# Performance work log

Measured on AMD Instinct MI355X. Metric: run time of the kernel, lower is better.

## Reference

```python
import jax, jax.numpy as jnp
import numpy as np

S, D, H, F = 4096, 1024, 16, 4096
DH = D // H  # 64
EPS = 1e-6


def _layer_norm(x, scale, bias):
    mu = jnp.mean(x, axis=-1, keepdims=True)
    var = jnp.mean(jnp.square(x - mu), axis=-1, keepdims=True)
    return (x - mu) * jax.lax.rsqrt(var + EPS) * scale + bias


def setup_inputs() -> dict:
    key = jax.random.key(0)
    ks = jax.random.split(key, 12)
    s = 0.02
    return {
        "x": jax.random.normal(ks[0], (S, D), jnp.float32),
        "Wq": jax.random.normal(ks[1], (D, H, DH), jnp.float32) * s,
        "bq": jnp.zeros((H, DH), jnp.float32),
        "Wk": jax.random.normal(ks[2], (D, H, DH), jnp.float32) * s,
        "bk": jnp.zeros((H, DH), jnp.float32),
        "Wv": jax.random.normal(ks[3], (D, H, DH), jnp.float32) * s,
        "bv": jnp.zeros((H, DH), jnp.float32),
        "Wo": jax.random.normal(ks[4], (H, DH, D), jnp.float32) * s,
        "bo": jnp.zeros((D,), jnp.float32),
        "ln1_scale": jnp.ones((D,), jnp.float32),
        "ln1_bias": jnp.zeros((D,), jnp.float32),
        "ln2_scale": jnp.ones((D,), jnp.float32),
        "ln2_bias": jnp.zeros((D,), jnp.float32),
        "W1": jax.random.normal(ks[5], (D, F), jnp.float32) * s,
        "b1": jnp.zeros((F,), jnp.float32),
        "W2": jax.random.normal(ks[6], (F, D), jnp.float32) * s,
        "b2": jnp.zeros((D,), jnp.float32),
    }


def reference(x, Wq, bq, Wk, bk, Wv, bv, Wo, bo,
              ln1_scale, ln1_bias, ln2_scale, ln2_bias,
              W1, b1, W2, b2):
    # --- attention block (pre-LN, no mask, no dropout, no RoPE) ---
    y = _layer_norm(x, ln1_scale, ln1_bias)            # [S, D]
    q = jnp.einsum("sd,dhk->shk", y, Wq) + bq          # [S, H, DH]
    k = jnp.einsum("sd,dhk->shk", y, Wk) + bk
    v = jnp.einsum("sd,dhk->shk", y, Wv) + bv
    scale = jnp.float32(1.0 / np.sqrt(DH))
    scores = jnp.einsum("qhd,khd->hqk", q * scale, k)  # [H, S, S]
    w = jax.nn.softmax(scores, axis=-1)
    ctx = jnp.einsum("hqk,khd->qhd", w, v)             # [S, H, DH]
    attn_out = jnp.einsum("qhd,hdo->qo", ctx, Wo) + bo  # [S, D]
    x = x + attn_out
    # --- FFN block ---
    y = _layer_norm(x, ln2_scale, ln2_bias)
    y = jax.nn.gelu(y @ W1 + b1, approximate=False)
    y = y @ W2 + b2
    return x + y
```

## Files before the change

### kernel.cpp

```cpp
#include <hip/hip_runtime.h>
#include <cstdint>
#include <cstddef>


typedef __attribute__((ext_vector_type(8))) __bf16 bf16x8;
typedef __attribute__((ext_vector_type(4))) float f32x4;
typedef __attribute__((ext_vector_type(2))) float f32x2;
typedef __attribute__((ext_vector_type(16))) float f32x16;
typedef __attribute__((ext_vector_type(4))) unsigned int u32x4;

__device__ inline unsigned short f2bf(float f) {
  unsigned int u = __float_as_uint(f);
  u += 0x7fffu + ((u >> 16) & 1u);
  return (unsigned short)(u >> 16);
}

__device__ inline void gload_lds16(const unsigned short* g, unsigned short* l) {
  __builtin_amdgcn_global_load_lds(
      (const __attribute__((address_space(1))) void*)g,
      (__attribute__((address_space(3))) void*)l, 16, 0, 0);
}

__global__ __launch_bounds__(256) void prep_all(
    const float* __restrict__ Wq, const float* __restrict__ Wk,
    const float* __restrict__ Wv, const float* __restrict__ Wo,
    const float* __restrict__ W1, const float* __restrict__ W2,
    const float* __restrict__ bq, const float* __restrict__ bk,
    const float* __restrict__ bv,
    const float* __restrict__ x, const float* __restrict__ g1,
    const float* __restrict__ be1, unsigned short* __restrict__ y1,
    unsigned short* __restrict__ WqkvT, unsigned short* __restrict__ WoT,
    unsigned short* __restrict__ W1T, unsigned short* __restrict__ W2T,
    float* __restrict__ bqkv) {
  int b = blockIdx.x;
  const int tid = threadIdx.x;
  if (b < 12) {
    int i = b * 256 + tid;
    bqkv[i] = (i < 1024) ? bq[i] : (i < 2048 ? bk[i - 1024] : bv[i - 2048]);
    return;
  }
  b -= 12;
  if (b < 4096) {
    const int row = b;
    const float4 v = ((const float4*)(x + (size_t)row * 1024))[tid];
    float s = v.x + v.y + v.z + v.w;
#pragma unroll
    for (int off = 1; off < 64; off <<= 1) s += __shfl_xor(s, off);
    __shared__ float red1[4], red2[4];
    int wave = tid >> 6;
    if ((tid & 63) == 0) red1[wave] = s;
    __syncthreads();
    float mu = (red1[0] + red1[1] + red1[2] + red1[3]) * (1.0f / 1024.0f);
    float dx = v.x - mu, dy = v.y - mu, dz = v.z - mu, dw = v.w - mu;
    float s2 = dx * dx + dy * dy + dz * dz + dw * dw;
#pragma unroll
    for (int off = 1; off < 64; off <<= 1) s2 += __shfl_xor(s2, off);
    if ((tid & 63) == 0) red2[wave] = s2;
    __syncthreads();
    float var = (red2[0] + red2[1] + red2[2] + red2[3]) * (1.0f / 1024.0f);
    float inv = rsqrtf(var + 1e-6f);
    int c = tid * 4;
    ushort4 o;
    o.x = f2bf(dx * inv * g1[c + 0] + be1[c + 0]);
    o.y = f2bf(dy * inv * g1[c + 1] + be1[c + 1]);
    o.z = f2bf(dz * inv * g1[c + 2] + be1[c + 2]);
    o.w = f2bf(dw * inv * g1[c + 3] + be1[c + 3]);
    ((ushort4*)(y1 + (size_t)row * 1024))[tid] = o;
    return;
  }
  b -= 4096;
  const float* in;
  unsigned short* out;
  int K, N, nbx;
  if (b < 4096) {
    const int sel = b >> 10;
    in = (sel == 0) ? Wq : (sel == 1) ? Wk : (sel == 2) ? Wv : Wo;
    out = (sel == 3) ? WoT : WqkvT + (size_t)sel * 1024 * 1024;
    K = 1024; N = 1024; nbx = 32; b &= 1023;
  } else if (b < 8192) {
    b -= 4096; in = W1; out = W1T; K = 1024; N = 4096; nbx = 128;
  } else {
    b -= 8192; in = W2; out = W2T; K = 4096; N = 1024; nbx = 32;
  }
  const int nb = (b % nbx) * 32, kb = (b / nbx) * 32;
  __shared__ float t[32][33];
  const int tx = tid & 31, ty = tid >> 5;
#pragma unroll
  for (int i = 0; i < 32; i += 8)
    t[ty + i][tx] = in[(size_t)(kb + ty + i) * N + nb + tx];
  __syncthreads();
#pragma unroll
  for (int i = 0; i < 32; i += 8)
    out[(size_t)(nb + ty + i) * K + kb + tx] = f2bf(t[tx][ty + i]);
}

__global__ __launch_bounds__(256) void ln_kernel(const float* __restrict__ x,
                                                 const float* __restrict__ gamma,
                                                 const float* __restrict__ beta,
                                                 unsigned short* __restrict__ y) {
  int row = blockIdx.x, tid = threadIdx.x;
  const float4 v = ((const float4*)(x + (size_t)row * 1024))[tid];
  float s = v.x + v.y + v.z + v.w;
#pragma unroll
  for (int off = 1; off < 64; off <<= 1) s += __shfl_xor(s, off);
  __shared__ float red1[4], red2[4];
  int wave = tid >> 6;
  if ((tid & 63) == 0) red1[wave] = s;
  __syncthreads();
  float mu = (red1[0] + red1[1] + red1[2] + red1[3]) * (1.0f / 1024.0f);
  float dx = v.x - mu, dy = v.y - mu, dz = v.z - mu, dw = v.w - mu;
  float s2 = dx * dx + dy * dy + dz * dz + dw * dw;
#pragma unroll
  for (int off = 1; off < 64; off <<= 1) s2 += __shfl_xor(s2, off);
  if ((tid & 63) == 0) red2[wave] = s2;
  __syncthreads();
  float var = (red2[0] + red2[1] + red2[2] + red2[3]) * (1.0f / 1024.0f);
  float inv = rsqrtf(var + 1e-6f);
  int c = tid * 4;
  ushort4 o;
  o.x = f2bf(dx * inv * gamma[c + 0] + beta[c + 0]);
  o.y = f2bf(dy * inv * gamma[c + 1] + beta[c + 1]);
  o.z = f2bf(dz * inv * gamma[c + 2] + beta[c + 2]);
  o.w = f2bf(dw * inv * gamma[c + 3] + beta[c + 3]);
  ((ushort4*)(y + (size_t)row * 1024))[tid] = o;
}

template <bool GELU, bool RES, bool OUTBF, bool SCALEQ>
__global__ __launch_bounds__(512, 2) void gemm8(
    const unsigned short* __restrict__ A,
    const unsigned short* __restrict__ BT,
    const float* __restrict__ bias,
    const float* __restrict__ res,
    void* __restrict__ out,
    int M, int N, int K) {
  constexpr int SLOT = 512 * 64;
  __shared__ unsigned short lds[2 * SLOT];
  (void)M;

  const int nbn = N / 256;
  const int bid = blockIdx.x;
  const int cpx = (int)gridDim.x >> 3;
  const int swzb = (bid & 7) * cpx + (bid >> 3);
  const int bm = swzb / nbn, bn = swzb % nbn;
  const int tid = threadIdx.x;
  const int lane = tid & 63, quad = lane >> 4, l16 = lane & 15;
  const int wm = tid >> 8, wn = (tid >> 6) & 3;

  const int rs = tid >> 3;
  const int xo = ((tid & 7) ^ (rs & 7)) * 8;
  const unsigned short* aSrc = A + (size_t)(bm * 256 + rs) * K + xo;
  const unsigned short* bSrc = BT + (size_t)(bn * 256 + rs) * K + xo;

  const int sw0 = (quad ^ (l16 & 7)) * 8;
  const int sw1 = ((quad ^ 4) ^ (l16 & 7)) * 8;
  const int aBase = (wm * 128 + l16) * 64;
  const int bBase = 16384 + (wn * 64 + l16) * 64;

  f32x4 acc[8][4];
  const f32x4 z4 = {0.f, 0.f, 0.f, 0.f};
#pragma unroll
  for (int i = 0; i < 8; ++i)
#pragma unroll
    for (int n = 0; n < 4; ++n) acc[i][n] = z4;

  const int NT = K >> 6;
  {
    unsigned short* dA = lds + (size_t)tid * 8;
    unsigned short* dB = lds + 16384 + (size_t)tid * 8;
#pragma unroll
    for (int u = 0; u < 4; ++u) gload_lds16(aSrc + (size_t)u * 64 * K, dA + u * 4096);
#pragma unroll
    for (int u = 0; u < 4; ++u) gload_lds16(bSrc + (size_t)u * 64 * K, dB + u * 4096);
  }

  for (int j = 0; j < NT; ++j) {
    const int s = j & 1;
    asm volatile("s_waitcnt vmcnt(0) lgkmcnt(0)" ::: "memory");
    __builtin_amdgcn_s_barrier();
    __builtin_amdgcn_sched_barrier(0);
    const unsigned short* Ts = lds + s * SLOT;
    unsigned short* stA = lds + (s ^ 1) * SLOT + (size_t)tid * 8;
    unsigned short* stB = stA + 16384;
    const bool pre = (j + 1 < NT);
    const int kN = (j + 1) << 6;

    bf16x8 af[4][2], bfr[4][2];
#pragma unroll
    for (int mm = 0; mm < 4; ++mm) {
      af[mm][0] = *(const bf16x8*)(Ts + aBase + mm * 1024 + sw0);
      af[mm][1] = *(const bf16x8*)(Ts + aBase + mm * 1024 + sw1);
    }
#pragma unroll
    for (int nn = 0; nn < 2; ++nn) {
      bfr[nn][0] = *(const bf16x8*)(Ts + bBase + nn * 1024 + sw0);
      bfr[nn][1] = *(const bf16x8*)(Ts + bBase + nn * 1024 + sw1);
    }
    if (pre) {
#pragma unroll
      for (int u = 0; u < 4; ++u)
        gload_lds16(aSrc + (size_t)u * 64 * K + kN, stA + u * 4096);
#pragma unroll
      for (int u = 0; u < 4; ++u)
        gload_lds16(bSrc + (size_t)u * 64 * K + kN, stB + u * 4096);
    }
    __builtin_amdgcn_s_barrier();
    __builtin_amdgcn_s_setprio(1);
#pragma unroll
    for (int mm = 0; mm < 4; ++mm)
#pragma unroll
      for (int nn = 0; nn < 2; ++nn) {
        acc[mm][nn] = __builtin_amdgcn_mfma_f32_16x16x32_bf16(af[mm][0], bfr[nn][0], acc[mm][nn], 0, 0, 0);
        acc[mm][nn] = __builtin_amdgcn_mfma_f32_16x16x32_bf16(af[mm][1], bfr[nn][1], acc[mm][nn], 0, 0, 0);
      }
    __builtin_amdgcn_s_setprio(0);
#pragma unroll
    for (int nn = 2; nn < 4; ++nn) {
      bfr[nn][0] = *(const bf16x8*)(Ts + bBase + nn * 1024 + sw0);
      bfr[nn][1] = *(const bf16x8*)(Ts + bBase + nn * 1024 + sw1);
    }
    __builtin_amdgcn_s_barrier();
    __builtin_amdgcn_s_setprio(1);
#pragma unroll
    for (int mm = 0; mm < 4; ++mm)
#pragma unroll
      for (int nn = 2; nn < 4; ++nn) {
        acc[mm][nn] = __builtin_amdgcn_mfma_f32_16x16x32_bf16(af[mm][0], bfr[nn][0], acc[mm][nn], 0, 0, 0);
        acc[mm][nn] = __builtin_amdgcn_mfma_f32_16x16x32_bf16(af[mm][1], bfr[nn][1], acc[mm][nn], 0, 0, 0);
      }
    __builtin_amdgcn_s_setprio(0);
#pragma unroll
    for (int mm = 0; mm < 4; ++mm) {
      af[mm][0] = *(const bf16x8*)(Ts + aBase + 4096 + mm * 1024 + sw0);
      af[mm][1] = *(const bf16x8*)(Ts + aBase + 4096 + mm * 1024 + sw1);
    }
    __builtin_amdgcn_s_barrier();
    __builtin_amdgcn_s_setprio(1);
#pragma unroll
    for (int mm = 0; mm < 4; ++mm)
#pragma unroll
      for (int nn = 0; nn < 2; ++nn) {
        acc[4 + mm][nn] = __builtin_amdgcn_mfma_f32_16x16x32_bf16(af[mm][0], bfr[nn][0], acc[4 + mm][nn], 0, 0, 0);
        acc[4 + mm][nn] = __builtin_amdgcn_mfma_f32_16x16x32_bf16(af[mm][1], bfr[nn][1], acc[4 + mm][nn], 0, 0, 0);
      }
    __builtin_amdgcn_s_setprio(0);
    __builtin_amdgcn_s_barrier();
    __builtin_amdgcn_s_setprio(1);
#pragma unroll
    for (int mm = 0; mm < 4; ++mm)
#pragma unroll
      for (int nn = 2; nn < 4; ++nn) {
        acc[4 + mm][nn] = __builtin_amdgcn_mfma_f32_16x16x32_bf16(af[mm][0], bfr[nn][0], acc[4 + mm][nn], 0, 0, 0);
        acc[4 + mm][nn] = __builtin_amdgcn_mfma_f32_16x16x32_bf16(af[mm][1], bfr[nn][1], acc[4 + mm][nn], 0, 0, 0);
      }
    __builtin_amdgcn_s_setprio(0);
  }

#pragma unroll
  for (int mi = 0; mi < 8; ++mi) {
    const int row0 = bm * 256 + wm * 128 + mi * 16 + quad * 4;
#pragma unroll
    for (int ni = 0; ni < 4; ++ni) {
      const int col = bn * 256 + wn * 64 + ni * 16 + l16;
      const float bv = bias[col];
      const float qs = (SCALEQ && col < 1024) ? 0.18033688f : 1.0f;
#pragma unroll
      for (int r = 0; r < 4; ++r) {
        float v = (acc[mi][ni][r] + bv) * qs;
        if (GELU) v = 0.5f * v * (1.0f + erff(v * 0.70710678118654752440f));
        if (RES) v += res[(size_t)(row0 + r) * N + col];
        if (OUTBF)
          ((unsigned short*)out)[(size_t)(row0 + r) * N + col] = f2bf(v);
        else
          ((float*)out)[(size_t)(row0 + r) * N + col] = v;
      }
    }
  }
}

template <bool GELU, bool RES, bool OUTBF>
__global__ __launch_bounds__(512, 2) void gemm3s(
    const unsigned short* __restrict__ A,
    const unsigned short* __restrict__ BT,
    const float* __restrict__ bias,
    const float* __restrict__ res,
    void* __restrict__ out,
    int M, int N, int K) {
  constexpr int SLOT = 256 * 64;
  __shared__ unsigned short lds[3 * SLOT];
  (void)M;

  const int nbn = N / 128;
  const int bid = blockIdx.x;
  const int cpx = (int)gridDim.x >> 3;
  const int swzb = (bid & 7) * cpx + (bid >> 3);
  const int bm = swzb / nbn, bn = swzb % nbn;
  const int tid = threadIdx.x;
  const int lane = tid & 63, quad = lane >> 4, l16 = lane & 15;
  const int wm = tid >> 8, wn = (tid >> 6) & 3;

  const int rs = tid >> 3;
  const int xo = ((tid & 7) ^ (rs & 7)) * 8;
  const unsigned short* aSrc = A + (size_t)(bm * 128 + rs) * K + xo;
  const unsigned short* bSrc = BT + (size_t)(bn * 128 + rs) * K + xo;

  const int sw0 = (quad ^ (l16 & 7)) * 8;
  const int sw1 = ((quad ^ 4) ^ (l16 & 7)) * 8;
  const int aBase = (wm * 64 + l16) * 64;
  const int bBase = 8192 + (wn * 32 + l16) * 64;

  f32x4 acc[4][2];
  const f32x4 z4 = {0.f, 0.f, 0.f, 0.f};
#pragma unroll
  for (int i = 0; i < 4; ++i)
#pragma unroll
    for (int n = 0; n < 2; ++n) acc[i][n] = z4;

  const int NT = K >> 6;
  {
    unsigned short* d0 = lds + (size_t)tid * 8;
    gload_lds16(aSrc, d0);
    gload_lds16(aSrc + (size_t)64 * K, d0 + 4096);
    gload_lds16(bSrc, d0 + 8192);
    gload_lds16(bSrc + (size_t)64 * K, d0 + 8192 + 4096);
    if (NT > 1) {
      unsigned short* d1 = lds + SLOT + (size_t)tid * 8;
      gload_lds16(aSrc + 64, d1);
      gload_lds16(aSrc + (size_t)64 * K + 64, d1 + 4096);
      gload_lds16(bSrc + 64, d1 + 8192);
      gload_lds16(bSrc + (size_t)64 * K + 64, d1 + 8192 + 4096);
    }
  }

  int sl = 0;
  for (int j = 0; j < NT; ++j) {
    if (j + 1 < NT)
      asm volatile("s_waitcnt vmcnt(4) lgkmcnt(0)" ::: "memory");
    else
      asm volatile("s_waitcnt vmcnt(0) lgkmcnt(0)" ::: "memory");
    __builtin_amdgcn_s_barrier();
    __builtin_amdgcn_sched_barrier(0);
    const unsigned short* Ts = lds + sl * SLOT;
    const int sl2 = (sl >= 1) ? sl - 1 : 2;
    unsigned short* st = lds + sl2 * SLOT + (size_t)tid * 8;

    bf16x8 af[2][2], bfr[2][2];
#pragma unroll
    for (int mm = 0; mm < 2; ++mm) {
      af[mm][0] = *(const bf16x8*)(Ts + aBase + mm * 1024 + sw0);
      af[mm][1] = *(const bf16x8*)(Ts + aBase + mm * 1024 + sw1);
    }
#pragma unroll
    for (int nn = 0; nn < 2; ++nn) {
      bfr[nn][0] = *(const bf16x8*)(Ts + bBase + nn * 1024 + sw0);
      bfr[nn][1] = *(const bf16x8*)(Ts + bBase + nn * 1024 + sw1);
    }
    if (j + 2 < NT) {
      const int kN = (j + 2) << 6;
      gload_lds16(aSrc + kN, st);
      gload_lds16(aSrc + (size_t)64 * K + kN, st + 4096);
      gload_lds16(bSrc + kN, st + 8192);
      gload_lds16(bSrc + (size_t)64 * K + kN, st + 8192 + 4096);
    }
    __builtin_amdgcn_s_barrier();
    __builtin_amdgcn_s_setprio(1);
#pragma unroll
    for (int mm = 0; mm < 2; ++mm)
#pragma unroll
      for (int nn = 0; nn < 2; ++nn) {
        acc[mm][nn] = __builtin_amdgcn_mfma_f32_16x16x32_bf16(af[mm][0], bfr[nn][0], acc[mm][nn], 0, 0, 0);
        acc[mm][nn] = __builtin_amdgcn_mfma_f32_16x16x32_bf16(af[mm][1], bfr[nn][1], acc[mm][nn], 0, 0, 0);
      }
    __builtin_amdgcn_s_setprio(0);
#pragma unroll
    for (int mm = 0; mm < 2; ++mm) {
      af[mm][0] = *(const bf16x8*)(Ts + aBase + 2048 + mm * 1024 + sw0);
      af[mm][1] = *(const bf16x8*)(Ts + aBase + 2048 + mm * 1024 + sw1);
    }
    __builtin_amdgcn_s_barrier();
    __builtin_amdgcn_s_setprio(1);
#pragma unroll
    for (int mm = 0; mm < 2; ++mm)
#pragma unroll
      for (int nn = 0; nn < 2; ++nn) {
        acc[2 + mm][nn] = __builtin_amdgcn_mfma_f32_16x16x32_bf16(af[mm][0], bfr[nn][0], acc[2 + mm][nn], 0, 0, 0);
        acc[2 + mm][nn] = __builtin_amdgcn_mfma_f32_16x16x32_bf16(af[mm][1], bfr[nn][1], acc[2 + mm][nn], 0, 0, 0);
      }
    __builtin_amdgcn_s_setprio(0);
    sl = (sl == 2) ? 0 : sl + 1;
  }

#pragma unroll
  for (int mi = 0; mi < 4; ++mi) {
    const int row0 = bm * 128 + wm * 64 + mi * 16 + quad * 4;
#pragma unroll
    for (int ni = 0; ni < 2; ++ni) {
      const int col = bn * 128 + wn * 32 + ni * 16 + l16;
      const float bv = bias[col];
#pragma unroll
      for (int r = 0; r < 4; ++r) {
        float v = acc[mi][ni][r] + bv;
        if (GELU) v = 0.5f * v * (1.0f + erff(v * 0.70710678118654752440f));
        if (RES) v += res[(size_t)(row0 + r) * N + col];
        if (OUTBF)
          ((unsigned short*)out)[(size_t)(row0 + r) * N + col] = f2bf(v);
        else
          ((float*)out)[(size_t)(row0 + r) * N + col] = v;
      }
    }
  }
}

__global__ __launch_bounds__(256) void prep_kv(const unsigned short* __restrict__ qkv,
                                               unsigned short* __restrict__ Kp,
                                               unsigned short* __restrict__ Vp) {
  __shared__ unsigned short Vt[64 * 64];
  int t = blockIdx.x, h = blockIdx.y;
  int tid = threadIdx.x;
  const int r2 = tid >> 3, c0 = (tid & 7) * 8;
  size_t tb = ((size_t)h * 64 + t) * 4096;
  {
    const unsigned short* kp = qkv + (size_t)(t * 64 + r2) * 3072 + 1024 + h * 64 + c0;
    uint4 k0 = *(const uint4*)kp;
    uint4 k1 = *(const uint4*)(kp + (size_t)32 * 3072);
    int c = c0 >> 3;
    *(uint4*)(Kp + tb + c * 512 + r2 * 8) = k0;
    *(uint4*)(Kp + tb + c * 512 + (r2 + 32) * 8) = k1;
  }
  {
    const unsigned short* vp = qkv + (size_t)(t * 64 + 2 * r2) * 3072 + 2048 + h * 64 + c0;
    uint4 v0 = *(const uint4*)vp;
    uint4 v1 = *(const uint4*)(vp + 3072);
    const unsigned short* p0 = (const unsigned short*)&v0;
    const unsigned short* p1 = (const unsigned short*)&v1;
#pragma unroll
    for (int dd = 0; dd < 8; dd++) {
      unsigned int pk = (unsigned int)p0[dd] | ((unsigned int)p1[dd] << 16);
      *(unsigned int*)&Vt[(c0 + dd) * 64 + 2 * r2] = pk;
    }
  }
  __syncthreads();
#pragma unroll
  for (int u0 = 0; u0 < 2; u0++) {
    int u = tid + u0 * 256;
    *(uint4*)(Vp + tb + u * 8) = *(const uint4*)&Vt[(u & 63) * 64 + (u >> 6) * 8];
  }
}

__global__ __launch_bounds__(256, 3) void attn_kernel(const unsigned short* __restrict__ qkv,
                                                      const unsigned short* __restrict__ Kp,
                                                      const unsigned short* __restrict__ Vp,
                                                      unsigned short* __restrict__ ctx) {
  __shared__ float lpw[4 * 32];
  int qt = blockIdx.x, h = blockIdx.y;
  int tid = threadIdx.x;
  int w = tid >> 6, lane = tid & 63;
  int l31 = lane & 31, hi = lane >> 5;

  bf16x8 qf[4];
  {
    const unsigned short* qp = qkv + (size_t)(qt * 128 + w * 32 + l31) * 3072 + h * 64 + hi * 8;
#pragma unroll
    for (int kk = 0; kk < 4; kk++) qf[kk] = *(const bf16x8*)(qp + kk * 16);
  }

  const size_t hb = (size_t)h * 64 * 4096;
  const unsigned short* kB = Kp + hb + hi * 512 + l31 * 8;
  const unsigned short* vB = Vp + hb + hi * 512 + l31 * 8;

  f32x16 accO0, accO1;
  f32x2 lp2 = {0.f, 0.f};
#pragma unroll
  for (int r = 0; r < 16; r++) { accO0[r] = 0.f; accO1[r] = 0.f; }

  bf16x8 kf[4];
#pragma unroll
  for (int kk = 0; kk < 4; kk++) kf[kk] = *(const bf16x8*)(kB + kk * 1024);

  for (int u = 0; u < 128; u++) {
    const unsigned short* vt = vB + (size_t)(u >> 1) * 4096 + (u & 1) * 2048;
    bf16x8 vA0 = *(const bf16x8*)(vt);
    bf16x8 vA1 = *(const bf16x8*)(vt + 1024);
    bf16x8 vB0 = *(const bf16x8*)(vt + 256);
    bf16x8 vB1 = *(const bf16x8*)(vt + 1024 + 256);

    f32x16 accS;
#pragma unroll
    for (int r = 0; r < 16; r++) accS[r] = 0.f;
#pragma unroll
    for (int kk = 0; kk < 4; kk++)
      accS = __builtin_amdgcn_mfma_f32_32x32x16_bf16(kf[kk], qf[kk], accS, 0, 0, 0);

    if (u < 127) {
      const int un = u + 1;
      const unsigned short* kt = kB + (size_t)(un >> 1) * 4096 + (un & 1) * 256;
#pragma unroll
      for (int kk = 0; kk < 4; kk++) kf[kk] = *(const bf16x8*)(kt + kk * 1024);
    }

    unsigned int pd[8];
#pragma unroll
    for (int i = 0; i < 8; i++) {
      float a = __builtin_amdgcn_exp2f(accS[2 * i]);
      float b = __builtin_amdgcn_exp2f(accS[2 * i + 1]);
      f32x2 ab = {a, b};
      lp2 += ab;
      pd[i] = __builtin_amdgcn_perm(__float_as_uint(b), __float_as_uint(a), 0x07060302);
    }
    asm("v_permlane32_swap_b32 %0, %1" : "+v"(pd[0]), "+v"(pd[2]));
    asm("v_permlane32_swap_b32 %0, %1" : "+v"(pd[1]), "+v"(pd[3]));
    asm("v_permlane32_swap_b32 %0, %1" : "+v"(pd[4]), "+v"(pd[6]));
    asm("v_permlane32_swap_b32 %0, %1" : "+v"(pd[5]), "+v"(pd[7]));
    u32x4 f0 = {pd[0], pd[1], pd[2], pd[3]};
    u32x4 f1 = {pd[4], pd[5], pd[6], pd[7]};
    bf16x8 pa0 = __builtin_bit_cast(bf16x8, f0);
    bf16x8 pa1 = __builtin_bit_cast(bf16x8, f1);

    accO0 = __builtin_amdgcn_mfma_f32_32x32x16_bf16(pa0, vA0, accO0, 0, 0, 0);
    accO1 = __builtin_amdgcn_mfma_f32_32x32x16_bf16(pa0, vB0, accO1, 0, 0, 0);
    accO0 = __builtin_amdgcn_mfma_f32_32x32x16_bf16(pa1, vA1, accO0, 0, 0, 0);
    accO1 = __builtin_amdgcn_mfma_f32_32x32x16_bf16(pa1, vB1, accO1, 0, 0, 0);
  }

  float lp = lp2.x + lp2.y;
  lp += __shfl_xor(lp, 32);
  if (hi == 0) lpw[w * 32 + l31] = lp;
  __syncthreads();
#pragma unroll
  for (int r = 0; r < 16; r++) {
    int q = (r & 3) + 8 * (r >> 2) + 4 * hi;
    float inv = 1.0f / lpw[w * 32 + q];
    int row = qt * 128 + w * 32 + q;
    size_t o = (size_t)row * 1024 + h * 64;
    ctx[o + l31] = f2bf(accO0[r] * inv);
    ctx[o + 32 + l31] = f2bf(accO1[r] * inv);
  }
}

extern "C" void kernel_launch(void* const* d_in, const int* in_sizes, int n_in,
                              void* d_out, int out_size, void* d_ws, size_t ws_size,
                              hipStream_t stream) {
  const float* x   = (const float*)d_in[0];
  const float* Wq  = (const float*)d_in[1];
  const float* bq  = (const float*)d_in[2];
  const float* Wk  = (const float*)d_in[3];
  const float* bk  = (const float*)d_in[4];
  const float* Wv  = (const float*)d_in[5];
  const float* bv  = (const float*)d_in[6];
  const float* Wo  = (const float*)d_in[7];
  const float* bo  = (const float*)d_in[8];
  const float* g1  = (const float*)d_in[9];
  const float* be1 = (const float*)d_in[10];
  const float* g2  = (const float*)d_in[11];
  const float* be2 = (const float*)d_in[12];
  const float* W1  = (const float*)d_in[13];
  const float* b1  = (const float*)d_in[14];
  const float* W2  = (const float*)d_in[15];
  const float* b2  = (const float*)d_in[16];
  float* out = (float*)d_out;

  char* p = (char*)d_ws;
  unsigned short* WqkvT = (unsigned short*)p; p += (size_t)3072 * 1024 * 2;
  unsigned short* WoT   = (unsigned short*)p; p += (size_t)1024 * 1024 * 2;
  unsigned short* W1T   = (unsigned short*)p; p += (size_t)4096 * 1024 * 2;
  unsigned short* W2T   = (unsigned short*)p; p += (size_t)1024 * 4096 * 2;
  float*          bqkv  = (float*)p;          p += 16384;
  unsigned short* y1    = (unsigned short*)p; p += (size_t)4096 * 1024 * 2;
  unsigned short* qkvb  = (unsigned short*)p; p += (size_t)4096 * 3072 * 2;
  unsigned short* ctxb  = (unsigned short*)p; p += (size_t)4096 * 1024 * 2;
  float*          x1    = (float*)p;          p += (size_t)4096 * 1024 * 4;
  unsigned short* Kp    = (unsigned short*)p; p += (size_t)16 * 64 * 4096 * 2;
  unsigned short* Vp    = (unsigned short*)p; p += (size_t)16 * 64 * 4096 * 2;
  unsigned short* hbuf  = qkvb;

  dim3 b256(256);
  dim3 b512(512);
  prep_all<<<dim3(16396), b256, 0, stream>>>(Wq, Wk, Wv, Wo, W1, W2, bq, bk, bv,
                                             x, g1, be1, y1,
                                             WqkvT, WoT, W1T, W2T, bqkv);

  gemm8<false, false, true, true><<<dim3(192), b512, 0, stream>>>(y1, WqkvT, bqkv, nullptr, qkvb, 4096, 3072, 1024);
  prep_kv<<<dim3(64, 16), b256, 0, stream>>>(qkvb, Kp, Vp);
  attn_kernel<<<dim3(32, 16), b256, 0, stream>>>(qkvb, Kp, Vp, ctxb);
  gemm3s<false, true, false><<<dim3(256), b512, 0, stream>>>(ctxb, WoT, bo, x, x1, 4096, 1024, 1024);
  ln_kernel<<<4096, b256, 0, stream>>>(x1, g2, be2, y1);
  gemm8<true, false, true, false><<<dim3(256), b512, 0, stream>>>(y1, W1T, b1, nullptr, hbuf, 4096, 4096, 1024);
  gemm3s<false, true, false><<<dim3(256), b512, 0, stream>>>(hbuf, W2T, b2, x1, out, 4096, 1024, 4096);
}
```

Before: 391.1 us.

## Replace N=1024 GEMMs with 128x64-tile 4-wave kernel and use polynomial GELU

The two GEMMs with N=1024 (out-projection and FFN down-projection) move from a 128x128-tile, 8-wave, triple-buffered kernel to a 128x64-tile, 4-wave, double-buffered kernel launched with 512 blocks. The aim is better CU coverage on the many-CU device and more resident blocks per CU, at the cost of less B-tile reuse and a full vmcnt(0) wait each iteration. Separately, the GELU epilogue in the FFN-up GEMM swaps erff for an Abramowitz-Stegun polynomial with __expf, which is cheaper but slightly approximate (error about 1e-7 abs).

```diff
diff --git a/kernel.cpp b/kernel.cpp
--- a/kernel.cpp
+++ b/kernel.cpp
@@ -13,6 +13,17 @@
   unsigned int u = __float_as_uint(f);
   u += 0x7fffu + ((u >> 16) & 1u);
   return (unsigned short)(u >> 16);
+}
+
+__device__ inline float gelu_f(float v) {
+  float z = v * 0.70710678118654752440f;
+  float az = fabsf(z);
+  float t = 1.0f / fmaf(0.3275911f, az, 1.0f);
+  float p = t * fmaf(t, fmaf(t, fmaf(t, fmaf(t, 1.061405429f, -1.453152027f),
+                                     1.421413741f), -0.284496736f), 0.254829592f);
+  float e = p * __expf(-az * az);
+  float erfz = copysignf(1.0f - e, z);
+  return 0.5f * v * (1.0f + erfz);
 }
 
 __device__ inline void gload_lds16(const unsigned short* g, unsigned short* l) {
@@ -266,7 +277,7 @@
 #pragma unroll
       for (int r = 0; r < 4; ++r) {
         float v = (acc[mi][ni][r] + bv) * qs;
-        if (GELU) v = 0.5f * v * (1.0f + erff(v * 0.70710678118654752440f));
+        if (GELU) v = gelu_f(v);
         if (RES) v += res[(size_t)(row0 + r) * N + col];
         if (OUTBF)
           ((unsigned short*)out)[(size_t)(row0 + r) * N + col] = f2bf(v);
@@ -277,31 +288,31 @@
   }
 }
 
-template <bool GELU, bool RES, bool OUTBF>
-__global__ __launch_bounds__(512, 2) void gemm3s(
+template <bool RES, bool OUTBF>
+__global__ __launch_bounds__(256, 3) void gemm4w(
     const unsigned short* __restrict__ A,
     const unsigned short* __restrict__ BT,
     const float* __restrict__ bias,
     const float* __restrict__ res,
     void* __restrict__ out,
     int M, int N, int K) {
-  constexpr int SLOT = 256 * 64;
-  __shared__ unsigned short lds[3 * SLOT];
+  constexpr int SLOT = 192 * 64;
+  __shared__ unsigned short lds[2 * SLOT];
   (void)M;
 
-  const int nbn = N / 128;
+  const int nbn = N / 64;
   const int bid = blockIdx.x;
   const int cpx = (int)gridDim.x >> 3;
   const int swzb = (bid & 7) * cpx + (bid >> 3);
   const int bm = swzb / nbn, bn = swzb % nbn;
   const int tid = threadIdx.x;
   const int lane = tid & 63, quad = lane >> 4, l16 = lane & 15;
-  const int wm = tid >> 8, wn = (tid >> 6) & 3;
+  const int wm = tid >> 7, wn = (tid >> 6) & 1;
 
   const int rs = tid >> 3;
   const int xo = ((tid & 7) ^ (rs & 7)) * 8;
   const unsigned short* aSrc = A + (size_t)(bm * 128 + rs) * K + xo;
-  const unsigned short* bSrc = BT + (size_t)(bn * 128 + rs) * K + xo;
+  const unsigned short* bSrc = BT + (size_t)(bn * 64 + rs) * K + xo;
 
   const int sw0 = (quad ^ (l16 & 7)) * 8;
   const int sw1 = ((quad ^ 4) ^ (l16 & 7)) * 8;
@@ -317,35 +328,24 @@
 
   const int NT = K >> 6;
   {
-    unsigned short* d0 = lds + (size_t)tid * 8;
-    gload_lds16(aSrc, d0);
-    gload_lds16(aSrc + (size_t)64 * K, d0 + 4096);
-    gload_lds16(bSrc, d0 + 8192);
-    gload_lds16(bSrc + (size_t)64 * K, d0 + 8192 + 4096);
-    if (NT > 1) {
-      unsigned short* d1 = lds + SLOT + (size_t)tid * 8;
-      gload_lds16(aSrc + 64, d1);
-      gload_lds16(aSrc + (size_t)64 * K + 64, d1 + 4096);
-      gload_lds16(bSrc + 64, d1 + 8192);
-      gload_lds16(bSrc + (size_t)64 * K + 64, d1 + 8192 + 4096);
-    }
-  }
-
-  int sl = 0;
+    unsigned short* d = lds + (size_t)tid * 8;
+#pragma unroll
+    for (int u = 0; u < 4; ++u) gload_lds16(aSrc + (size_t)u * 32 * K, d + u * 2048);
+#pragma unroll
+    for (int u = 0; u < 2; ++u) gload_lds16(bSrc + (size_t)u * 32 * K, d + 8192 + u * 2048);
+  }
+
   for (int j = 0; j < NT; ++j) {
-    if (j + 1 < NT)
-      asm volatile("s_waitcnt vmcnt(4) lgkmcnt(0)" ::: "memory");
-    else
-      asm volatile("s_waitcnt vmcnt(0) lgkmcnt(0)" ::: "memory");
+    const int s = j & 1;
+    asm volatile("s_waitcnt vmcnt(0) lgkmcnt(0)" ::: "memory");
     __builtin_amdgcn_s_barrier();
     __builtin_amdgcn_sched_barrier(0);
-    const unsigned short* Ts = lds + sl * SLOT;
-    const int sl2 = (sl >= 1) ? sl - 1 : 2;
-    unsigned short* st = lds + sl2 * SLOT + (size_t)tid * 8;
-
-    bf16x8 af[2][2], bfr[2][2];
-#pragma unroll
-    for (int mm = 0; mm < 2; ++mm) {
+    const unsigned short* Ts = lds + s * SLOT;
+    unsigned short* st = lds + (s ^ 1) * SLOT + (size_t)tid * 8;
+
+    bf16x8 af[4][2], bfr[2][2];
+#pragma unroll
+    for (int mm = 0; mm < 4; ++mm) {
       af[mm][0] = *(const bf16x8*)(Ts + aBase + mm * 1024 + sw0);
       af[mm][1] = *(const bf16x8*)(Ts + aBase + mm * 1024 + sw1);
     }
@@ -354,39 +354,23 @@
       bfr[nn][0] = *(const bf16x8*)(Ts + bBase + nn * 1024 + sw0);
       bfr[nn][1] = *(const bf16x8*)(Ts + bBase + nn * 1024 + sw1);
     }
-    if (j + 2 < NT) {
-      const int kN = (j + 2) << 6;
-      gload_lds16(aSrc + kN, st);
-      gload_lds16(aSrc + (size_t)64 * K + kN, st + 4096);
-      gload_lds16(bSrc + kN, st + 8192);
-      gload_lds16(bSrc + (size_t)64 * K + kN, st + 8192 + 4096);
+    if (j + 1 < NT) {
+      const int kN = (j + 1) << 6;
+#pragma unroll
+      for (int u = 0; u < 4; ++u) gload_lds16(aSrc + (size_t)u * 32 * K + kN, st + u * 2048);
+#pragma unroll
+      for (int u = 0; u < 2; ++u) gload_lds16(bSrc + (size_t)u * 32 * K + kN, st + 8192 + u * 2048);
     }
     __builtin_amdgcn_s_barrier();
     __builtin_amdgcn_s_setprio(1);
 #pragma unroll
-    for (int mm = 0; mm < 2; ++mm)
+    for (int mm = 0; mm < 4; ++mm)
 #pragma unroll
       for (int nn = 0; nn < 2; ++nn) {
         acc[mm][nn] = __builtin_amdgcn_mfma_f32_16x16x32_bf16(af[mm][0], bfr[nn][0], acc[mm][nn], 0, 0, 0);
         acc[mm][nn] = __builtin_amdgcn_mfma_f32_16x16x32_bf16(af[mm][1], bfr[nn][1], acc[mm][nn], 0, 0, 0);
       }
     __builtin_amdgcn_s_setprio(0);
-#pragma unroll
-    for (int mm = 0; mm < 2; ++mm) {
-      af[mm][0] = *(const bf16x8*)(Ts + aBase + 2048 + mm * 1024 + sw0);
-      af[mm][1] = *(const bf16x8*)(Ts + aBase + 2048 + mm * 1024 + sw1);
-    }
-    __builtin_amdgcn_s_barrier();
-    __builtin_amdgcn_s_setprio(1);
-#pragma unroll
-    for (int mm = 0; mm < 2; ++mm)
-#pragma unroll
-      for (int nn = 0; nn < 2; ++nn) {
-        acc[2 + mm][nn] = __builtin_amdgcn_mfma_f32_16x16x32_bf16(af[mm][0], bfr[nn][0], acc[2 + mm][nn], 0, 0, 0);
-        acc[2 + mm][nn] = __builtin_amdgcn_mfma_f32_16x16x32_bf16(af[mm][1], bfr[nn][1], acc[2 + mm][nn], 0, 0, 0);
-      }
-    __builtin_amdgcn_s_setprio(0);
-    sl = (sl == 2) ? 0 : sl + 1;
   }
 
 #pragma unroll
@@ -394,12 +378,11 @@
     const int row0 = bm * 128 + wm * 64 + mi * 16 + quad * 4;
 #pragma unroll
     for (int ni = 0; ni < 2; ++ni) {
-      const int col = bn * 128 + wn * 32 + ni * 16 + l16;
+      const int col = bn * 64 + wn * 32 + ni * 16 + l16;
       const float bv = bias[col];
 #pragma unroll
       for (int r = 0; r < 4; ++r) {
         float v = acc[mi][ni][r] + bv;
-        if (GELU) v = 0.5f * v * (1.0f + erff(v * 0.70710678118654752440f));
         if (RES) v += res[(size_t)(row0 + r) * N + col];
         if (OUTBF)
           ((unsigned short*)out)[(size_t)(row0 + r) * N + col] = f2bf(v);
@@ -581,8 +564,8 @@
   gemm8<false, false, true, true><<<dim3(192), b512, 0, stream>>>(y1, WqkvT, bqkv, nullptr, qkvb, 4096, 3072, 1024);
   prep_kv<<<dim3(64, 16), b256, 0, stream>>>(qkvb, Kp, Vp);
   attn_kernel<<<dim3(32, 16), b256, 0, stream>>>(qkvb, Kp, Vp, ctxb);
-  gemm3s<false, true, false><<<dim3(256), b512, 0, stream>>>(ctxb, WoT, bo, x, x1, 4096, 1024, 1024);
+  gemm4w<true, false><<<dim3(512), b256, 0, stream>>>(ctxb, WoT, bo, x, x1, 4096, 1024, 1024);
   ln_kernel<<<4096, b256, 0, stream>>>(x1, g2, be2, y1);
   gemm8<true, false, true, false><<<dim3(256), b512, 0, stream>>>(y1, W1T, b1, nullptr, hbuf, 4096, 4096, 1024);
-  gemm3s<false, true, false><<<dim3(256), b512, 0, stream>>>(hbuf, W2T, b2, x1, out, 4096, 1024, 4096);
-}
+  gemm4w<true, false><<<dim3(512), b256, 0, stream>>>(hbuf, W2T, b2, x1, out, 4096, 1024, 4096);
+}
```

Result: faster. 361.2 us (-7.7%).
